# Kernel tuning notes

Hardware: AMD Instinct MI355X
Metric: run time of the kernel (lower is better)

Reference implementation:

```python
import jax, jax.numpy as jnp
import numpy as np

ROPE_BASE = 10000.0

def rope_tables(n, r):
    inv = 1.0 / (ROPE_BASE ** (jnp.arange(0, r, 2, dtype=jnp.float32) / r))  # [r/2]
    ang = jnp.arange(n, dtype=jnp.float32)[:, None] * inv[None, :]           # [n, r/2]
    cos = jnp.concatenate([jnp.cos(ang), jnp.cos(ang)], axis=-1)             # [n, r]
    sin = jnp.concatenate([jnp.sin(ang), jnp.sin(ang)], axis=-1)
    return cos, sin

def apply_rope(x, cos, sin):
    # x: [B, H, T, r]; cos/sin: [T, r]
    half = x.shape[-1] // 2
    x_rot = jnp.concatenate([-x[..., half:], x[..., :half]], axis=-1)
    return x * cos + x_rot * sin

def setup_inputs() -> dict:
    key = jax.random.key(0)
    ks = jax.random.split(key, 8)
    B, S, L = 2, 1024, 1024
    dim_q, h, k, d_c, d_cq, r = 2048, 16, 128, 512, 1536, 64
    w = 0.02  # weight scale to keep activations numerically tame
    return {
        'hidden_q': jax.random.normal(ks[0], (B, S, dim_q), jnp.float32),
        'kv_c':     jax.random.normal(ks[1], (B, L, d_c), jnp.float32),
        'Wq':       jax.random.normal(ks[2], (h * k, dim_q), jnp.float32) * w,
        'w_kc_q':   jax.random.normal(ks[3], (h, k, d_cq), jnp.float32) * w,
        'W_qr':     jax.random.normal(ks[4], (h, d_cq, r), jnp.float32) * (w / np.sqrt(r)),
        'W_kr':     jax.random.normal(ks[5], (h, d_c, r), jnp.float32) * w,
        'w_kc_kv':  jax.random.normal(ks[6], (h, k, d_c), jnp.float32) * w,
        'Wo':       jax.random.normal(ks[7], (dim_q, h * k), jnp.float32) * w,
    }

def reference(hidden_q, kv_c, Wq, w_kc_q, W_qr, W_kr, w_kc_kv, Wo):
    B, S, _ = hidden_q.shape
    L = kv_c.shape[1]
    h, k, _ = w_kc_q.shape
    r = W_qr.shape[-1]
    # q projection: [B,S,h,k]
    q_hk = (hidden_q @ Wq.T).reshape(B, S, h, k)
    # low-rank expand to q-compressed space then retrieval space
    q_big = jnp.einsum('bshk,hkq->bshq', q_hk, w_kc_q)          # [B,S,h,d_cq]
    q_r = jnp.einsum('bshq,hqr->bhsr', q_big, W_qr)             # [B,h,S,r]
    k_r = jnp.einsum('bld,hdr->bhlr', kv_c, W_kr)               # [B,h,L,r]
    cos_S, sin_S = rope_tables(S, r)
    cos_L, sin_L = rope_tables(L, r)
    q_r = apply_rope(q_r, cos_S, sin_S)
    k_r = apply_rope(k_r, cos_L, sin_L)
    # attention in retrieval space, values are compressed kv (shared across heads)
    scores = jnp.einsum('bhsr,bhlr->bhsl', q_r, k_r)            # scale baked into W_qr
    attn = jax.nn.softmax(scores, axis=-1)
    ctx_c = jnp.einsum('bhsl,bld->bhsd', attn, kv_c)            # [B,h,S,d_c]
    # decompress per head: w_kc_kv is [h,k,d_c]
    ctx_lat = jnp.einsum('bhsd,hkd->bshk', ctx_c, w_kc_kv).reshape(B, S, h * k)
    return ctx_lat @ Wo.T
```

## Files before the change

### kernel.cpp

```cpp
#include <hip/hip_runtime.h>
#include <math.h>
#include <stdint.h>


typedef __attribute__((ext_vector_type(8))) short short8;
typedef __attribute__((ext_vector_type(4))) float f32x4;

#define GLOAD16(gsrc, ldst)                                                            \
  __builtin_amdgcn_global_load_lds((const __attribute__((address_space(1))) void*)(gsrc), \
                                   (__attribute__((address_space(3))) void*)(ldst), 16, 0, 0)

__device__ inline uint16_t f2b(float x) {
  uint32_t u = __builtin_bit_cast(uint32_t, x);
  u += 0x7fff + ((u >> 16) & 1);
  return (uint16_t)(u >> 16);
}
__device__ inline float b2f(uint16_t b) {
  uint32_t u = ((uint32_t)b) << 16;
  return __builtin_bit_cast(float, u);
}
__device__ inline uint32_t cvtpk_bf16(float lo, float hi) {
  uint32_t d;
  asm("v_cvt_pk_bf16_f32 %0, %1, %2" : "=v"(d) : "v"(lo), "v"(hi));
  return d;
}

__global__ __launch_bounds__(256) void prep_kernel(
    const float* __restrict__ s0, uint16_t* __restrict__ t0, const float* __restrict__ s1,
    uint16_t* __restrict__ t1, const float* __restrict__ s2, uint16_t* __restrict__ t2,
    const float* __restrict__ s3, uint16_t* __restrict__ t3, const float* __restrict__ s4,
    uint16_t* __restrict__ t4, float* __restrict__ cosK, float* __restrict__ sinK,
    float* __restrict__ cosQ, float* __restrict__ sinQ, const float* __restrict__ Wq,
    uint16_t* __restrict__ WqT, const float* __restrict__ W_qr, uint16_t* __restrict__ WqrT,
    const float* __restrict__ W_kr, uint16_t* __restrict__ WkrT) {
  __shared__ float t[32][33];
  int bid = blockIdx.x;
  if (bid >= 6912) {
    int tb = bid - 6912;
    const float* src;
    uint16_t* dst;
    int R, C, r0, c0;
    if (tb < 4096) {
      src = Wq; dst = WqT; R = 2048; C = 2048;
      r0 = (tb & 63) * 32; c0 = (tb >> 6) * 32;
    } else if (tb < 5632) {
      int b = tb - 4096;
      int z = b / 96, rem = b % 96;
      src = W_qr + (size_t)z * 98304; dst = WqrT + (size_t)z * 98304;
      R = 1536; C = 64;
      r0 = (rem >> 1) * 32; c0 = (rem & 1) * 32;
    } else {
      int b = tb - 5632;
      int z = b / 32, rem = b % 32;
      src = W_kr + (size_t)z * 32768; dst = WkrT + (size_t)z * 32768;
      R = 512; C = 64;
      r0 = (rem >> 1) * 32; c0 = (rem & 1) * 32;
    }
    int tr = threadIdx.x >> 5, tc = threadIdx.x & 31;
#pragma unroll
    for (int i = 0; i < 4; ++i) t[tr + i * 8][tc] = src[(size_t)(r0 + tr + i * 8) * C + c0 + tc];
    __syncthreads();
#pragma unroll
    for (int i = 0; i < 4; ++i)
      dst[(size_t)(c0 + tr + i * 8) * R + r0 + tc] = f2b(t[tc][tr + i * 8]);
    return;
  }
  if (bid >= 6656) {
    const float LOG2E = 1.44269504088896341f;
    int idx = (bid - 6656) * 256 + threadIdx.x;
    int s = idx >> 6, j = idx & 63;
    int i = j & 31;
    float inv = powf(10000.0f, -(float)(2 * i) / 64.0f);
    float ang = (float)s * inv;
    float c = cosf(ang), sn = sinf(ang);
    cosK[idx] = c;
    sinK[idx] = sn;
    cosQ[idx] = c * LOG2E;
    sinQ[idx] = sn * LOG2E;
    return;
  }
  const float* s;
  uint16_t* tt;
  int off;
  if (bid < 2048) { s = s0; tt = t0; off = bid; }
  else if (bid < 2560) { s = s1; tt = t1; off = bid - 2048; }
  else if (bid < 3072) { s = s2; tt = t2; off = bid - 2560; }
  else if (bid < 5120) { s = s3; tt = t3; off = bid - 3072; }
  else { s = s4; tt = t4; off = bid - 5120; }
  int i = off * 256 + threadIdx.x;
  const float4* s4v = (const float4*)s;
  float4 a = s4v[i * 2], b = s4v[i * 2 + 1];
  union {
    uint16_t u[8];
    uint4 v;
  } o;
  o.u[0] = f2b(a.x); o.u[1] = f2b(a.y); o.u[2] = f2b(a.z); o.u[3] = f2b(a.w);
  o.u[4] = f2b(b.x); o.u[5] = f2b(b.y); o.u[6] = f2b(b.z); o.u[7] = f2b(b.w);
  ((uint4*)tt)[i] = o.v;
}

template <int BM, int EPI, int SPLITK = 1>
__global__ __launch_bounds__(256) void gemm_mfma_kernel(const uint16_t* __restrict__ A,
                                                        const uint16_t* __restrict__ Bt,
                                                        void* __restrict__ Cv, int K, int lda,
                                                        int ldb, int ldc, int aZ, int bZ,
                                                        int cZ) {
  constexpr int MT = BM / 32;
  __shared__ __align__(16) uint16_t As[2][BM * 64];
  __shared__ __align__(16) uint16_t Bs[2][128 * 64];
  int z = blockIdx.z;
  if (SPLITK > 1) {
    int zh = z / SPLITK, zk = z % SPLITK;
    A += (size_t)zh * aZ + (size_t)zk * K;
    Bt += (size_t)zh * bZ + (size_t)zk * K;
  } else {
    A += (size_t)z * aZ;
    Bt += (size_t)z * bZ;
  }
  int m0 = blockIdx.x * BM, n0 = blockIdx.y * 128;
  int tid = threadIdx.x;
  int wave = tid >> 6, lane = tid & 63;
  int wm = wave >> 1, wn = wave & 1;
  int rS = lane >> 3, sl = lane & 7;
  int lr = lane >> 4, lc = lane & 15;

  auto stage = [&](int k0, int buf) {
#pragma unroll
    for (int i = 0; i < MT; ++i) {
      int idx = wave * MT + i;
      int row = idx * 8 + rS;
      GLOAD16(A + (size_t)(m0 + row) * lda + k0 + ((sl ^ (row & 7)) << 3),
              (uint8_t*)As[buf] + idx * 1024);
    }
#pragma unroll
    for (int i = 0; i < 4; ++i) {
      int idx = wave * 4 + i;
      int row = idx * 8 + rS;
      GLOAD16(Bt + (size_t)(n0 + row) * ldb + k0 + ((sl ^ (row & 7)) << 3),
              (uint8_t*)Bs[buf] + idx * 1024);
    }
  };

  f32x4 acc[MT][4] = {};
  stage(0, 0);
  int cur = 0;
  for (int k0 = 0; k0 < K; k0 += 64) {
    __syncthreads();
    if (k0 + 64 < K) stage(k0 + 64, cur ^ 1);
    short8 af[MT][2], bf[4][2];
#pragma unroll
    for (int t = 0; t < MT; ++t)
#pragma unroll
      for (int ks = 0; ks < 2; ++ks) {
        int slot = ks * 4 + lr;
        int ra = wm * (BM / 2) + t * 16 + lc;
        af[t][ks] =
            *(const short8*)((const uint8_t*)As[cur] + ra * 128 + ((slot ^ (ra & 7)) << 4));
      }
#pragma unroll
    for (int t = 0; t < 4; ++t)
#pragma unroll
      for (int ks = 0; ks < 2; ++ks) {
        int slot = ks * 4 + lr;
        int rb = wn * 64 + t * 16 + lc;
        bf[t][ks] =
            *(const short8*)((const uint8_t*)Bs[cur] + rb * 128 + ((slot ^ (rb & 7)) << 4));
      }
    __builtin_amdgcn_s_setprio(1);
#pragma unroll
    for (int mt = 0; mt < MT; ++mt)
#pragma unroll
      for (int nt = 0; nt < 4; ++nt) {
        acc[mt][nt] =
            __builtin_amdgcn_mfma_f32_16x16x32_bf16(af[mt][0], bf[nt][0], acc[mt][nt], 0, 0, 0);
        acc[mt][nt] =
            __builtin_amdgcn_mfma_f32_16x16x32_bf16(af[mt][1], bf[nt][1], acc[mt][nt], 0, 0, 0);
      }
    __builtin_amdgcn_s_setprio(0);
    cur ^= 1;
  }
#pragma unroll
  for (int mt = 0; mt < MT; ++mt)
#pragma unroll
    for (int nt = 0; nt < 4; ++nt)
#pragma unroll
      for (int r = 0; r < 4; ++r) {
        int m = m0 + wm * (BM / 2) + mt * 16 + lr * 4 + r;
        int n = n0 + wn * 64 + nt * 16 + lc;
        float v = acc[mt][nt][r];
        if (EPI == 0)
          ((float*)Cv)[(size_t)z * cZ + (size_t)m * ldc + n] = v;
        else
          ((uint16_t*)Cv)[(size_t)z * cZ + (size_t)m * ldc + n] = f2b(v);
      }
}

__global__ __launch_bounds__(256) void fold2_kernel(const float* __restrict__ tmp1,
                                                    const uint16_t* __restrict__ WqT,
                                                    uint16_t* __restrict__ WfoldT) {
  __shared__ __align__(16) uint16_t As[2][64 * 64];
  __shared__ __align__(16) uint16_t Bs[2][128 * 64];
  int z = blockIdx.z;
  int n0 = blockIdx.y * 128;
  const uint16_t* Bt = WqT + z * 128;
  int tid = threadIdx.x;
  int wave = tid >> 6, lane = tid & 63;
  int wm = wave >> 1, wn = wave & 1;
  int rS = lane >> 3, sl = lane & 7;
  int lr = lane >> 4, lc = lane & 15;

  {
    int row = tid >> 2;
    int kbase = (tid & 3) * 32;
    const float* tp = tmp1 + (size_t)z * 32768 + row * 128;
#pragma unroll
    for (int c = 0; c < 8; ++c) {
      int k4 = kbase + c * 4;
      float4 s = *(const float4*)(tp + k4);
      float4 s1 = *(const float4*)(tp + 8192 + k4);
      float4 s2 = *(const float4*)(tp + 16384 + k4);
      float4 s3 = *(const float4*)(tp + 24576 + k4);
      s.x = ((s.x + s1.x) + s2.x) + s3.x;
      s.y = ((s.y + s1.y) + s2.y) + s3.y;
      s.z = ((s.z + s1.z) + s2.z) + s3.z;
      s.w = ((s.w + s1.w) + s2.w) + s3.w;
      uint32_t lo = cvtpk_bf16(s.x, s.y);
      uint32_t hi = cvtpk_bf16(s.z, s.w);
      int buf = k4 >> 6, kl = k4 & 63;
      int slot = kl >> 3;
      uint32_t addr = row * 128 + ((slot ^ (row & 7)) << 4) + (kl & 7) * 2;
      *(uint32_t*)((uint8_t*)As[buf] + addr) = lo;
      *(uint32_t*)((uint8_t*)As[buf] + addr + 4) = hi;
    }
  }

  auto stageB = [&](int k0, int buf) {
#pragma unroll
    for (int i = 0; i < 4; ++i) {
      int idx = wave * 4 + i;
      int row = idx * 8 + rS;
      GLOAD16(Bt + (size_t)(n0 + row) * 2048 + k0 + ((sl ^ (row & 7)) << 3),
              (uint8_t*)Bs[buf] + idx * 1024);
    }
  };

  f32x4 acc[2][4] = {};
  stageB(0, 0);
  int cur = 0;
  for (int k0 = 0; k0 < 128; k0 += 64) {
    __syncthreads();
    if (k0 + 64 < 128) stageB(64, 1);
    short8 af[2][2], bf[4][2];
#pragma unroll
    for (int t = 0; t < 2; ++t)
#pragma unroll
      for (int ks = 0; ks < 2; ++ks) {
        int slot = ks * 4 + lr;
        int ra = wm * 32 + t * 16 + lc;
        af[t][ks] =
            *(const short8*)((const uint8_t*)As[cur] + ra * 128 + ((slot ^ (ra & 7)) << 4));
      }
#pragma unroll
    for (int t = 0; t < 4; ++t)
#pragma unroll
      for (int ks = 0; ks < 2; ++ks) {
        int slot = ks * 4 + lr;
        int rb = wn * 64 + t * 16 + lc;
        bf[t][ks] =
            *(const short8*)((const uint8_t*)Bs[cur] + rb * 128 + ((slot ^ (rb & 7)) << 4));
      }
    __builtin_amdgcn_s_setprio(1);
#pragma unroll
    for (int mt = 0; mt < 2; ++mt)
#pragma unroll
      for (int nt = 0; nt < 4; ++nt) {
        acc[mt][nt] =
            __builtin_amdgcn_mfma_f32_16x16x32_bf16(af[mt][0], bf[nt][0], acc[mt][nt], 0, 0, 0);
        acc[mt][nt] =
            __builtin_amdgcn_mfma_f32_16x16x32_bf16(af[mt][1], bf[nt][1], acc[mt][nt], 0, 0, 0);
      }
    __builtin_amdgcn_s_setprio(0);
    cur ^= 1;
  }
#pragma unroll
  for (int mt = 0; mt < 2; ++mt)
#pragma unroll
    for (int nt = 0; nt < 4; ++nt)
#pragma unroll
      for (int r = 0; r < 4; ++r) {
        int m = wm * 32 + mt * 16 + lr * 4 + r;
        int n = n0 + wn * 64 + nt * 16 + lc;
        WfoldT[(size_t)z * 131072 + (size_t)m * 2048 + n] = f2b(acc[mt][nt][r]);
      }
}

__global__ __launch_bounds__(256) void gemm_triple_kernel(
    const uint16_t* __restrict__ hqb, const uint16_t* __restrict__ WfoldT,
    uint16_t* __restrict__ qrb, const uint16_t* __restrict__ kvb,
    const uint16_t* __restrict__ WkrT, uint16_t* __restrict__ krb,
    const uint16_t* __restrict__ wkvb, uint16_t* __restrict__ VhT,
    const float* __restrict__ cosQ, const float* __restrict__ sinQ,
    const float* __restrict__ cosK, const float* __restrict__ sinK) {
  __shared__ __align__(16) uint16_t As[2][64 * 64];
  __shared__ __align__(16) uint16_t Bs[2][128 * 64];
  int bx = blockIdx.x, byr = blockIdx.y;
  const uint16_t *A, *Bt;
  uint16_t* Cv;
  const float *rc, *rs;
  int K, lda, ldb, n0, mode;
  if (byr < 8) {
    A = hqb; Bt = WfoldT; Cv = qrb; K = 2048; lda = 2048; ldb = 2048;
    n0 = byr * 128; mode = 0; rc = cosQ; rs = sinQ;
  } else if (byr < 16) {
    A = kvb; Bt = WkrT; Cv = krb; K = 512; lda = 512; ldb = 512;
    n0 = (byr - 8) * 128; mode = 0; rc = cosK; rs = sinK;
  } else {
    A = kvb; Bt = wkvb; Cv = VhT; K = 512; lda = 512; ldb = 512;
    n0 = (byr - 16) * 128; mode = 1; rc = nullptr; rs = nullptr;
  }
  int m0 = bx * 64;
  int tid = threadIdx.x;
  int wave = tid >> 6, lane = tid & 63;
  int wm = wave >> 1, wn = wave & 1;
  int rS = lane >> 3, sl = lane & 7;
  int lr = lane >> 4, lc = lane & 15;

  auto stage = [&](int k0, int buf) {
#pragma unroll
    for (int i = 0; i < 2; ++i) {
      int idx = wave * 2 + i;
      int row = idx * 8 + rS;
      GLOAD16(A + (size_t)(m0 + row) * lda + k0 + ((sl ^ (row & 7)) << 3),
              (uint8_t*)As[buf] + idx * 1024);
    }
#pragma unroll
    for (int i = 0; i < 4; ++i) {
      int idx = wave * 4 + i;
      int row = idx * 8 + rS;
      GLOAD16(Bt + (size_t)(n0 + row) * ldb + k0 + ((sl ^ (row & 7)) << 3),
              (uint8_t*)Bs[buf] + idx * 1024);
    }
  };

  f32x4 acc[2][4] = {};
  stage(0, 0);
  int cur = 0;
  for (int k0 = 0; k0 < K; k0 += 64) {
    __syncthreads();
    if (k0 + 64 < K) stage(k0 + 64, cur ^ 1);
    short8 af[2][2], bf[4][2];
#pragma unroll
    for (int t = 0; t < 2; ++t)
#pragma unroll
      for (int ks = 0; ks < 2; ++ks) {
        int slot = ks * 4 + lr;
        int ra = wm * 32 + t * 16 + lc;
        af[t][ks] =
            *(const short8*)((const uint8_t*)As[cur] + ra * 128 + ((slot ^ (ra & 7)) << 4));
      }
#pragma unroll
    for (int t = 0; t < 4; ++t)
#pragma unroll
      for (int ks = 0; ks < 2; ++ks) {
        int slot = ks * 4 + lr;
        int rb = wn * 64 + t * 16 + lc;
        bf[t][ks] =
            *(const short8*)((const uint8_t*)Bs[cur] + rb * 128 + ((slot ^ (rb & 7)) << 4));
      }
    __builtin_amdgcn_s_setprio(1);
#pragma unroll
    for (int mt = 0; mt < 2; ++mt)
#pragma unroll
      for (int nt = 0; nt < 4; ++nt) {
        acc[mt][nt] =
            __builtin_amdgcn_mfma_f32_16x16x32_bf16(af[mt][0], bf[nt][0], acc[mt][nt], 0, 0, 0);
        acc[mt][nt] =
            __builtin_amdgcn_mfma_f32_16x16x32_bf16(af[mt][1], bf[nt][1], acc[mt][nt], 0, 0, 0);
      }
    __builtin_amdgcn_s_setprio(0);
    cur ^= 1;
  }
  if (mode == 0) {
#pragma unroll
    for (int mt = 0; mt < 2; ++mt)
#pragma unroll
      for (int nt = 0; nt < 4; ++nt)
#pragma unroll
        for (int r = 0; r < 4; ++r) {
          int m = m0 + wm * 32 + mt * 16 + lr * 4 + r;
          int n = n0 + wn * 64 + nt * 16 + lc;
          int pos = m & 1023, j = n & 63;
          float x = acc[mt][nt][r];
          float prt = acc[mt][nt ^ 2][r];
          float rot = (nt & 2) ? prt : -prt;
          float v = fmaf(x, rc[pos * 64 + j], rot * rs[pos * 64 + j]);
          Cv[(size_t)m * 1024 + n] = f2b(v);
        }
  } else {
#pragma unroll
    for (int mt = 0; mt < 2; ++mt)
#pragma unroll
      for (int nt = 0; nt < 4; ++nt)
#pragma unroll
        for (int r = 0; r < 4; ++r) {
          int m = m0 + wm * 32 + mt * 16 + lr * 4 + r;
          int n = n0 + wn * 64 + nt * 16 + lc;
          Cv[((size_t)((m >> 10) * 2048 + n)) * 1024 + (m & 1023)] = f2b(acc[mt][nt][r]);
        }
  }
}

__global__ __launch_bounds__(512, 2) void flash3_kernel(const uint16_t* __restrict__ qrb,
                                                        const uint16_t* __restrict__ krb,
                                                        const uint16_t* __restrict__ VhT,
                                                        uint16_t* __restrict__ ctxlatb) {
  __shared__ __align__(16) uint8_t lds[67584];
  int bh = blockIdx.x;
  int b = bh >> 4, h = bh & 15;
  int s0 = blockIdx.y * 128;
  int tid = threadIdx.x, wave = tid >> 6, lane = tid & 63;
  int lr = lane >> 4, lc = lane & 15;
  int rS = lane >> 3, sl = lane & 7;

  uint8_t* Ps = lds + 49152 + wave * 2304;

  const uint16_t* qrow = qrb + (size_t)(b * 1024 + s0 + wave * 16 + lc) * 1024 + h * 64;
  short8 qa[2];
  qa[0] = *(const short8*)(qrow + lr * 8);
  qa[1] = *(const short8*)(qrow + 32 + lr * 8);

  float l_run = 0.f;
  f32x4 o[8] = {};

  uint8_t* psW = Ps + lc * 144 + lr * 8;
  const uint8_t* psR = Ps + lc * 144 + lr * 16;

  const uint16_t* krbase = krb + (size_t)(b * 1024) * 1024 + h * 64;
  const uint16_t* vtbase = VhT + (size_t)(b * 2048 + h * 128) * 1024;

  auto stageKV = [&](int l0, int buf) {
#pragma unroll
    for (int i = 0; i < 3; ++i) {
      int g = wave * 3 + i;
      if (g < 8) {
        int row = g * 8 + rS;
        GLOAD16(krbase + (size_t)(l0 + row) * 1024 + ((sl ^ (row & 7)) << 3),
                lds + buf * 8192 + g * 1024);
      } else {
        int v = g - 8;
        int row = v * 8 + rS;
        GLOAD16(vtbase + (size_t)row * 1024 + l0 + ((sl ^ (row & 7)) << 3),
                lds + 16384 + buf * 16384 + v * 1024);
      }
    }
  };

  stageKV(0, 0);
  int cur = 0;
  for (int t = 0; t < 16; ++t) {
    __syncthreads();
    if (t < 15) stageKV((t + 1) * 64, cur ^ 1);
    const uint8_t* Ks = lds + cur * 8192;
    const uint8_t* Vs = lds + 16384 + cur * 16384;

    f32x4 sc[4];
    __builtin_amdgcn_s_setprio(1);
#pragma unroll
    for (int nt = 0; nt < 4; ++nt) {
      int rowk = nt * 16 + lc;
      short8 kb0 = *(const short8*)(Ks + rowk * 128 + ((lr ^ (rowk & 7)) << 4));
      short8 kb1 = *(const short8*)(Ks + rowk * 128 + (((4 + lr) ^ (rowk & 7)) << 4));
      f32x4 z = {};
      z = __builtin_amdgcn_mfma_f32_16x16x32_bf16(kb0, qa[0], z, 0, 0, 0);
      sc[nt] = __builtin_amdgcn_mfma_f32_16x16x32_bf16(kb1, qa[1], z, 0, 0, 0);
    }
    __builtin_amdgcn_s_setprio(0);

    float ps = 0.f;
#pragma unroll
    for (int nt = 0; nt < 4; ++nt) {
#pragma unroll
      for (int rp = 0; rp < 2; ++rp) {
        float p0 = exp2f(sc[nt][rp * 2] - 8.0f);
        float p1 = exp2f(sc[nt][rp * 2 + 1] - 8.0f);
        ps += p0 + p1;
        *(uint32_t*)(psW + nt * 32 + rp * 4) = cvtpk_bf16(p0, p1);
      }
    }
    l_run += ps;

    short8 pa[2];
    pa[0] = *(const short8*)(psR);
    pa[1] = *(const short8*)(psR + 64);
    __builtin_amdgcn_s_setprio(1);
#pragma unroll
    for (int nt = 0; nt < 8; ++nt) {
      int rowv = nt * 16 + lc;
      short8 vb0 = *(const short8*)(Vs + rowv * 128 + ((lr ^ (rowv & 7)) << 4));
      short8 vb1 = *(const short8*)(Vs + rowv * 128 + (((4 + lr) ^ (rowv & 7)) << 4));
      o[nt] = __builtin_amdgcn_mfma_f32_16x16x32_bf16(pa[0], vb0, o[nt], 0, 0, 0);
      o[nt] = __builtin_amdgcn_mfma_f32_16x16x32_bf16(pa[1], vb1, o[nt], 0, 0, 0);
    }
    __builtin_amdgcn_s_setprio(0);
    cur ^= 1;
  }

  l_run += __shfl_xor(l_run, 16);
  l_run += __shfl_xor(l_run, 32);
  float li[4];
#pragma unroll
  for (int r = 0; r < 4; ++r) li[r] = 1.0f / __shfl(l_run, lr * 4 + r);
  uint16_t* orow = ctxlatb + (size_t)(b * 1024 + s0 + wave * 16) * 2048 + h * 128;
#pragma unroll
  for (int nt = 0; nt < 8; ++nt)
#pragma unroll
    for (int r = 0; r < 4; ++r)
      orow[(size_t)(lr * 4 + r) * 2048 + nt * 16 + lc] = f2b(o[nt][r] * li[r]);
}

extern "C" void kernel_launch(void* const* d_in, const int* in_sizes, int n_in,
                              void* d_out, int out_size, void* d_ws, size_t ws_size,
                              hipStream_t stream) {
  const float* hidden_q = (const float*)d_in[0];
  const float* kv_c = (const float*)d_in[1];
  const float* Wq = (const float*)d_in[2];
  const float* w_kc_q = (const float*)d_in[3];
  const float* W_qr = (const float*)d_in[4];
  const float* W_kr = (const float*)d_in[5];
  const float* w_kc_kv = (const float*)d_in[6];
  const float* Wo = (const float*)d_in[7];
  float* out = (float*)d_out;

  const size_t MB = 1024 * 1024;
  uint8_t* base = (uint8_t*)d_ws;
  uint16_t* Wob = (uint16_t*)(base + 0 * MB);
  uint16_t* qrb = (uint16_t*)(base + 8 * MB);
  uint16_t* krb = (uint16_t*)(base + 12 * MB);
  uint16_t* VhT = (uint16_t*)(base + 16 * MB);
  uint16_t* ctxlatb = (uint16_t*)(base + 24 * MB);
  float* cosK = (float*)(base + 32 * MB);
  float* sinK = (float*)(base + 32 * MB + 262144);
  float* cosQ = (float*)(base + 32 * MB + 524288);
  float* sinQ = (float*)(base + 32 * MB + 786432);
  uint16_t* hqb = (uint16_t*)(base + 33 * MB);
  uint16_t* kvb = (uint16_t*)(base + 41 * MB);
  uint16_t* wkvb = (uint16_t*)(base + 43 * MB);
  uint16_t* WqT = (uint16_t*)(base + 45 * MB);
  uint16_t* WqrT = (uint16_t*)(base + 53 * MB);
  uint16_t* wkcqb = (uint16_t*)(base + 56 * MB);
  float* tmp1 = (float*)(base + 62 * MB);
  uint16_t* WkrT = (uint16_t*)(base + 64 * MB + 262144);

  prep_kernel<<<dim3(13056), dim3(256), 0, stream>>>(
      hidden_q, hqb, kv_c, kvb, w_kc_kv, wkvb, Wo, Wob, w_kc_q, wkcqb, cosK, sinK, cosQ, sinQ, Wq,
      WqT, (const float*)W_qr, WqrT, (const float*)W_kr, WkrT);
  gemm_mfma_kernel<64, 0, 4><<<dim3(1, 1, 64), dim3(256), 0, stream>>>(
      WqrT, wkcqb, tmp1, 384, 1536, 1536, 128, 98304, 196608, 8192);
  uint16_t* WfoldT = wkcqb;
  fold2_kernel<<<dim3(1, 16, 16), dim3(256), 0, stream>>>(tmp1, WqT, WfoldT);
  gemm_triple_kernel<<<dim3(32, 32), dim3(256), 0, stream>>>(
      hqb, WfoldT, qrb, kvb, WkrT, krb, wkvb, VhT, cosQ, sinQ, cosK, sinK);
  flash3_kernel<<<dim3(32, 8), dim3(512), 0, stream>>>(qrb, krb, VhT, ctxlatb);
  gemm_mfma_kernel<64, 0><<<dim3(32, 16), dim3(256), 0, stream>>>(ctxlatb, Wob, out, 2048, 2048,
                                                                  2048, 2048, 0, 0, 0);
}
```

Before: 129.0 us.

## Fuse fp32-to-bf16 conversion of hidden_q and Wo into GEMM loaders; deepen split-K

The separate prep-kernel conversion passes for hidden_q and Wo are removed. Those fp32 tensors are now loaded directly inside the q-projection and output GEMMs and packed to bf16 while staging into LDS, using a new dedicated output GEMM kernel with tile swizzling. The weight-fold split-K goes from 4 to 8 partitions, and prep conversion now uses packed cvt instructions. This cuts a round trip of bf16 intermediates through global memory, but the GEMM loaders now read twice the bytes synchronously instead of using async global-to-LDS loads.

```diff
diff --git a/kernel.cpp b/kernel.cpp
--- a/kernel.cpp
+++ b/kernel.cpp
@@ -15,10 +15,6 @@
   u += 0x7fff + ((u >> 16) & 1);
   return (uint16_t)(u >> 16);
 }
-__device__ inline float b2f(uint16_t b) {
-  uint32_t u = ((uint32_t)b) << 16;
-  return __builtin_bit_cast(float, u);
-}
 __device__ inline uint32_t cvtpk_bf16(float lo, float hi) {
   uint32_t d;
   asm("v_cvt_pk_bf16_f32 %0, %1, %2" : "=v"(d) : "v"(lo), "v"(hi));
@@ -26,17 +22,16 @@
 }
 
 __global__ __launch_bounds__(256) void prep_kernel(
-    const float* __restrict__ s0, uint16_t* __restrict__ t0, const float* __restrict__ s1,
-    uint16_t* __restrict__ t1, const float* __restrict__ s2, uint16_t* __restrict__ t2,
-    const float* __restrict__ s3, uint16_t* __restrict__ t3, const float* __restrict__ s4,
-    uint16_t* __restrict__ t4, float* __restrict__ cosK, float* __restrict__ sinK,
-    float* __restrict__ cosQ, float* __restrict__ sinQ, const float* __restrict__ Wq,
-    uint16_t* __restrict__ WqT, const float* __restrict__ W_qr, uint16_t* __restrict__ WqrT,
-    const float* __restrict__ W_kr, uint16_t* __restrict__ WkrT) {
+    const float* __restrict__ s1, uint16_t* __restrict__ t1, const float* __restrict__ s2,
+    uint16_t* __restrict__ t2, const float* __restrict__ s4, uint16_t* __restrict__ t4,
+    float* __restrict__ cosK, float* __restrict__ sinK, float* __restrict__ cosQ,
+    float* __restrict__ sinQ, const float* __restrict__ Wq, uint16_t* __restrict__ WqT,
+    const float* __restrict__ W_qr, uint16_t* __restrict__ WqrT, const float* __restrict__ W_kr,
+    uint16_t* __restrict__ WkrT) {
   __shared__ float t[32][33];
   int bid = blockIdx.x;
-  if (bid >= 6912) {
-    int tb = bid - 6912;
+  if (bid >= 2816) {
+    int tb = bid - 2816;
     const float* src;
     uint16_t* dst;
     int R, C, r0, c0;
@@ -65,9 +60,9 @@
       dst[(size_t)(c0 + tr + i * 8) * R + r0 + tc] = f2b(t[tc][tr + i * 8]);
     return;
   }
-  if (bid >= 6656) {
+  if (bid >= 2560) {
     const float LOG2E = 1.44269504088896341f;
-    int idx = (bid - 6656) * 256 + threadIdx.x;
+    int idx = (bid - 2560) * 256 + threadIdx.x;
     int s = idx >> 6, j = idx & 63;
     int i = j & 31;
     float inv = powf(10000.0f, -(float)(2 * i) / 64.0f);
@@ -82,21 +77,18 @@
   const float* s;
   uint16_t* tt;
   int off;
-  if (bid < 2048) { s = s0; tt = t0; off = bid; }
-  else if (bid < 2560) { s = s1; tt = t1; off = bid - 2048; }
-  else if (bid < 3072) { s = s2; tt = t2; off = bid - 2560; }
-  else if (bid < 5120) { s = s3; tt = t3; off = bid - 3072; }
-  else { s = s4; tt = t4; off = bid - 5120; }
+  if (bid < 512) { s = s1; tt = t1; off = bid; }
+  else if (bid < 1024) { s = s2; tt = t2; off = bid - 512; }
+  else { s = s4; tt = t4; off = bid - 1024; }
   int i = off * 256 + threadIdx.x;
   const float4* s4v = (const float4*)s;
   float4 a = s4v[i * 2], b = s4v[i * 2 + 1];
-  union {
-    uint16_t u[8];
-    uint4 v;
-  } o;
-  o.u[0] = f2b(a.x); o.u[1] = f2b(a.y); o.u[2] = f2b(a.z); o.u[3] = f2b(a.w);
-  o.u[4] = f2b(b.x); o.u[5] = f2b(b.y); o.u[6] = f2b(b.z); o.u[7] = f2b(b.w);
-  ((uint4*)tt)[i] = o.v;
+  uint4 v;
+  v.x = cvtpk_bf16(a.x, a.y);
+  v.y = cvtpk_bf16(a.z, a.w);
+  v.z = cvtpk_bf16(b.x, b.y);
+  v.w = cvtpk_bf16(b.z, b.w);
+  ((uint4*)tt)[i] = v;
 }
 
 template <int BM, int EPI, int SPLITK = 1>
@@ -212,18 +204,19 @@
   {
     int row = tid >> 2;
     int kbase = (tid & 3) * 32;
-    const float* tp = tmp1 + (size_t)z * 32768 + row * 128;
+    const float* tp = tmp1 + (size_t)z * 65536 + row * 128;
 #pragma unroll
     for (int c = 0; c < 8; ++c) {
       int k4 = kbase + c * 4;
       float4 s = *(const float4*)(tp + k4);
-      float4 s1 = *(const float4*)(tp + 8192 + k4);
-      float4 s2 = *(const float4*)(tp + 16384 + k4);
-      float4 s3 = *(const float4*)(tp + 24576 + k4);
-      s.x = ((s.x + s1.x) + s2.x) + s3.x;
-      s.y = ((s.y + s1.y) + s2.y) + s3.y;
-      s.z = ((s.z + s1.z) + s2.z) + s3.z;
-      s.w = ((s.w + s1.w) + s2.w) + s3.w;
+#pragma unroll
+      for (int p = 1; p < 8; ++p) {
+        float4 sp = *(const float4*)(tp + p * 8192 + k4);
+        s.x += sp.x;
+        s.y += sp.y;
+        s.z += sp.z;
+        s.w += sp.w;
+      }
       uint32_t lo = cvtpk_bf16(s.x, s.y);
       uint32_t hi = cvtpk_bf16(s.z, s.w);
       int buf = k4 >> 6, kl = k4 & 63;
@@ -295,7 +288,7 @@
 }
 
 __global__ __launch_bounds__(256) void gemm_triple_kernel(
-    const uint16_t* __restrict__ hqb, const uint16_t* __restrict__ WfoldT,
+    const float* __restrict__ hidden_q, const uint16_t* __restrict__ WfoldT,
     uint16_t* __restrict__ qrb, const uint16_t* __restrict__ kvb,
     const uint16_t* __restrict__ WkrT, uint16_t* __restrict__ krb,
     const uint16_t* __restrict__ wkvb, uint16_t* __restrict__ VhT,
@@ -304,18 +297,19 @@
   __shared__ __align__(16) uint16_t As[2][64 * 64];
   __shared__ __align__(16) uint16_t Bs[2][128 * 64];
   int bx = blockIdx.x, byr = blockIdx.y;
-  const uint16_t *A, *Bt;
+  const uint16_t *Abf = nullptr, *Bt;
   uint16_t* Cv;
   const float *rc, *rs;
-  int K, lda, ldb, n0, mode;
+  int K, ldb, n0, mode;
+  bool aF32 = false;
   if (byr < 8) {
-    A = hqb; Bt = WfoldT; Cv = qrb; K = 2048; lda = 2048; ldb = 2048;
+    aF32 = true; Bt = WfoldT; Cv = qrb; K = 2048; ldb = 2048;
     n0 = byr * 128; mode = 0; rc = cosQ; rs = sinQ;
   } else if (byr < 16) {
-    A = kvb; Bt = WkrT; Cv = krb; K = 512; lda = 512; ldb = 512;
+    Abf = kvb; Bt = WkrT; Cv = krb; K = 512; ldb = 512;
     n0 = (byr - 8) * 128; mode = 0; rc = cosK; rs = sinK;
   } else {
-    A = kvb; Bt = wkvb; Cv = VhT; K = 512; lda = 512; ldb = 512;
+    Abf = kvb; Bt = wkvb; Cv = VhT; K = 512; ldb = 512;
     n0 = (byr - 16) * 128; mode = 1; rc = nullptr; rs = nullptr;
   }
   int m0 = bx * 64;
@@ -326,12 +320,29 @@
   int lr = lane >> 4, lc = lane & 15;
 
   auto stage = [&](int k0, int buf) {
-#pragma unroll
-    for (int i = 0; i < 2; ++i) {
-      int idx = wave * 2 + i;
-      int row = idx * 8 + rS;
-      GLOAD16(A + (size_t)(m0 + row) * lda + k0 + ((sl ^ (row & 7)) << 3),
-              (uint8_t*)As[buf] + idx * 1024);
+    if (aF32) {
+#pragma unroll
+      for (int i = 0; i < 2; ++i) {
+        int task = tid * 2 + i;
+        int row = task >> 3, c = task & 7;
+        const float* src = hidden_q + (size_t)(m0 + row) * 2048 + k0 + c * 8;
+        float4 a = *(const float4*)src;
+        float4 b = *(const float4*)(src + 4);
+        uint4 v;
+        v.x = cvtpk_bf16(a.x, a.y);
+        v.y = cvtpk_bf16(a.z, a.w);
+        v.z = cvtpk_bf16(b.x, b.y);
+        v.w = cvtpk_bf16(b.z, b.w);
+        *(uint4*)((uint8_t*)As[buf] + row * 128 + ((c ^ (row & 7)) << 4)) = v;
+      }
+    } else {
+#pragma unroll
+      for (int i = 0; i < 2; ++i) {
+        int idx = wave * 2 + i;
+        int row = idx * 8 + rS;
+        GLOAD16(Abf + (size_t)(m0 + row) * 512 + k0 + ((sl ^ (row & 7)) << 3),
+                (uint8_t*)As[buf] + idx * 1024);
+      }
     }
 #pragma unroll
     for (int i = 0; i < 4; ++i) {
@@ -408,6 +419,94 @@
           Cv[((size_t)((m >> 10) * 2048 + n)) * 1024 + (m & 1023)] = f2b(acc[mt][nt][r]);
         }
   }
+}
+
+__global__ __launch_bounds__(256) void gemm_out_kernel(const uint16_t* __restrict__ A,
+                                                       const float* __restrict__ Wo,
+                                                       float* __restrict__ C) {
+  __shared__ __align__(16) uint16_t As[2][64 * 64];
+  __shared__ __align__(16) uint16_t Bs[2][128 * 64];
+  int lin = blockIdx.x + 32 * blockIdx.y;
+  int swz = (lin & 7) * 64 + (lin >> 3);
+  int m0 = (swz & 31) * 64, n0 = (swz >> 5) * 128;
+  int tid = threadIdx.x;
+  int wave = tid >> 6, lane = tid & 63;
+  int wm = wave >> 1, wn = wave & 1;
+  int rS = lane >> 3, sl = lane & 7;
+  int lr = lane >> 4, lc = lane & 15;
+
+  auto stage = [&](int k0, int buf) {
+#pragma unroll
+    for (int i = 0; i < 2; ++i) {
+      int idx = wave * 2 + i;
+      int row = idx * 8 + rS;
+      GLOAD16(A + (size_t)(m0 + row) * 2048 + k0 + ((sl ^ (row & 7)) << 3),
+              (uint8_t*)As[buf] + idx * 1024);
+    }
+#pragma unroll
+    for (int i = 0; i < 4; ++i) {
+      int task = tid * 4 + i;
+      int row = task >> 3, c = task & 7;
+      const float* src = Wo + (size_t)(n0 + row) * 2048 + k0 + c * 8;
+      float4 a = *(const float4*)src;
+      float4 b = *(const float4*)(src + 4);
+      uint4 v;
+      v.x = cvtpk_bf16(a.x, a.y);
+      v.y = cvtpk_bf16(a.z, a.w);
+      v.z = cvtpk_bf16(b.x, b.y);
+      v.w = cvtpk_bf16(b.z, b.w);
+      *(uint4*)((uint8_t*)Bs[buf] + row * 128 + ((c ^ (row & 7)) << 4)) = v;
+    }
+  };
+
+  f32x4 acc[2][4] = {};
+  stage(0, 0);
+  int cur = 0;
+  for (int k0 = 0; k0 < 2048; k0 += 64) {
+    __syncthreads();
+    if (k0 + 64 < 2048) stage(k0 + 64, cur ^ 1);
+    short8 af[2][2], bf[4][2];
+#pragma unroll
+    for (int t = 0; t < 2; ++t)
+#pragma unroll
+      for (int ks = 0; ks < 2; ++ks) {
+        int slot = ks * 4 + lr;
+        int ra = wm * 32 + t * 16 + lc;
+        af[t][ks] =
+            *(const short8*)((const uint8_t*)As[cur] + ra * 128 + ((slot ^ (ra & 7)) << 4));
+      }
+#pragma unroll
+    for (int t = 0; t < 4; ++t)
+#pragma unroll
+      for (int ks = 0; ks < 2; ++ks) {
+        int slot = ks * 4 + lr;
+        int rb = wn * 64 + t * 16 + lc;
+        bf[t][ks] =
+            *(const short8*)((const uint8_t*)Bs[cur] + rb * 128 + ((slot ^ (rb & 7)) << 4));
+      }
+    __builtin_amdgcn_s_setprio(1);
+#pragma unroll
+    for (int mt = 0; mt < 2; ++mt)
+#pragma unroll
+      for (int nt = 0; nt < 4; ++nt) {
+        acc[mt][nt] =
+            __builtin_amdgcn_mfma_f32_16x16x32_bf16(af[mt][0], bf[nt][0], acc[mt][nt], 0, 0, 0);
+        acc[mt][nt] =
+            __builtin_amdgcn_mfma_f32_16x16x32_bf16(af[mt][1], bf[nt][1], acc[mt][nt], 0, 0, 0);
+      }
+    __builtin_amdgcn_s_setprio(0);
+    cur ^= 1;
+  }
+#pragma unroll
+  for (int mt = 0; mt < 2; ++mt)
+#pragma unroll
+    for (int nt = 0; nt < 4; ++nt)
+#pragma unroll
+      for (int r = 0; r < 4; ++r) {
+        int m = m0 + wm * 32 + mt * 16 + lr * 4 + r;
+        int n = n0 + wn * 64 + nt * 16 + lc;
+        C[(size_t)m * 2048 + n] = acc[mt][nt][r];
+      }
 }
 
 __global__ __launch_bounds__(512, 2) void flash3_kernel(const uint16_t* __restrict__ qrb,
@@ -533,34 +632,31 @@
 
   const size_t MB = 1024 * 1024;
   uint8_t* base = (uint8_t*)d_ws;
-  uint16_t* Wob = (uint16_t*)(base + 0 * MB);
-  uint16_t* qrb = (uint16_t*)(base + 8 * MB);
-  uint16_t* krb = (uint16_t*)(base + 12 * MB);
-  uint16_t* VhT = (uint16_t*)(base + 16 * MB);
-  uint16_t* ctxlatb = (uint16_t*)(base + 24 * MB);
-  float* cosK = (float*)(base + 32 * MB);
-  float* sinK = (float*)(base + 32 * MB + 262144);
-  float* cosQ = (float*)(base + 32 * MB + 524288);
-  float* sinQ = (float*)(base + 32 * MB + 786432);
-  uint16_t* hqb = (uint16_t*)(base + 33 * MB);
-  uint16_t* kvb = (uint16_t*)(base + 41 * MB);
-  uint16_t* wkvb = (uint16_t*)(base + 43 * MB);
-  uint16_t* WqT = (uint16_t*)(base + 45 * MB);
-  uint16_t* WqrT = (uint16_t*)(base + 53 * MB);
-  uint16_t* wkcqb = (uint16_t*)(base + 56 * MB);
-  float* tmp1 = (float*)(base + 62 * MB);
-  uint16_t* WkrT = (uint16_t*)(base + 64 * MB + 262144);
-
-  prep_kernel<<<dim3(13056), dim3(256), 0, stream>>>(
-      hidden_q, hqb, kv_c, kvb, w_kc_kv, wkvb, Wo, Wob, w_kc_q, wkcqb, cosK, sinK, cosQ, sinQ, Wq,
-      WqT, (const float*)W_qr, WqrT, (const float*)W_kr, WkrT);
-  gemm_mfma_kernel<64, 0, 4><<<dim3(1, 1, 64), dim3(256), 0, stream>>>(
-      WqrT, wkcqb, tmp1, 384, 1536, 1536, 128, 98304, 196608, 8192);
+  uint16_t* qrb = (uint16_t*)(base + 0 * MB);
+  uint16_t* krb = (uint16_t*)(base + 4 * MB);
+  uint16_t* VhT = (uint16_t*)(base + 8 * MB);
+  uint16_t* ctxlatb = (uint16_t*)(base + 16 * MB);
+  float* cosK = (float*)(base + 24 * MB);
+  float* sinK = (float*)(base + 24 * MB + 262144);
+  float* cosQ = (float*)(base + 24 * MB + 524288);
+  float* sinQ = (float*)(base + 24 * MB + 786432);
+  uint16_t* kvb = (uint16_t*)(base + 25 * MB);
+  uint16_t* wkvb = (uint16_t*)(base + 27 * MB);
+  uint16_t* WqT = (uint16_t*)(base + 29 * MB);
+  uint16_t* WqrT = (uint16_t*)(base + 37 * MB);
+  uint16_t* wkcqb = (uint16_t*)(base + 40 * MB);
+  float* tmp1 = (float*)(base + 46 * MB);
+  uint16_t* WkrT = (uint16_t*)(base + 50 * MB);
+
+  prep_kernel<<<dim3(8960), dim3(256), 0, stream>>>(kv_c, kvb, w_kc_kv, wkvb, w_kc_q, wkcqb, cosK,
+                                                    sinK, cosQ, sinQ, Wq, WqT, (const float*)W_qr,
+                                                    WqrT, (const float*)W_kr, WkrT);
+  gemm_mfma_kernel<64, 0, 8><<<dim3(1, 1, 128), dim3(256), 0, stream>>>(
+      WqrT, wkcqb, tmp1, 192, 1536, 1536, 128, 98304, 196608, 8192);
   uint16_t* WfoldT = wkcqb;
   fold2_kernel<<<dim3(1, 16, 16), dim3(256), 0, stream>>>(tmp1, WqT, WfoldT);
   gemm_triple_kernel<<<dim3(32, 32), dim3(256), 0, stream>>>(
-      hqb, WfoldT, qrb, kvb, WkrT, krb, wkvb, VhT, cosQ, sinQ, cosK, sinK);
+      hidden_q, WfoldT, qrb, kvb, WkrT, krb, wkvb, VhT, cosQ, sinQ, cosK, sinK);
   flash3_kernel<<<dim3(32, 8), dim3(512), 0, stream>>>(qrb, krb, VhT, ctxlatb);
-  gemm_mfma_kernel<64, 0><<<dim3(32, 16), dim3(256), 0, stream>>>(ctxlatb, Wob, out, 2048, 2048,
-                                                                  2048, 2048, 0, 0, 0);
-}
+  gemm_out_kernel<<<dim3(32, 16), dim3(256), 0, stream>>>(ctxlatb, Wo, out);
+}
```

Measured after the change: 181.7 us. +40.9%, slower.
